# Kernel tuning notes

Hardware: AMD Instinct MI355X
Metric: run time of the kernel (lower is better)

## Reference

```python
import jax, jax.numpy as jnp
import numpy as np

DIM = 1024
HEADS = 16
DIM_HEAD = 64
INNER = HEADS * DIM_HEAD  # 1024
SCALE = DIM ** (-0.5)  # module scales by dim**-0.5 (not dim_head)


def setup_inputs() -> dict:
    key = jax.random.key(0)
    kx, kqkv, kwo, kbo = jax.random.split(key, 4)
    x = jax.random.normal(kx, (2, 2048, DIM), dtype=jnp.float32)
    W_qkv = jax.random.normal(kqkv, (DIM, 3 * INNER), dtype=jnp.float32) * (DIM ** -0.5)
    W_out = jax.random.normal(kwo, (INNER, DIM), dtype=jnp.float32) * (INNER ** -0.5)
    b_out = jax.random.normal(kbo, (DIM,), dtype=jnp.float32) * 0.01
    return {"x": x, "W_qkv": W_qkv, "W_out": W_out, "b_out": b_out}


def reference(x, W_qkv, W_out, b_out):
    b, n, _ = x.shape
    qkv = x @ W_qkv  # [b, n, 3*inner]
    q, k, v = jnp.split(qkv, 3, axis=-1)
    # [b, n, h*d] -> [b, h, n, d]
    reshape = lambda t: t.reshape(b, n, HEADS, DIM_HEAD).transpose(0, 2, 1, 3)
    q, k, v = reshape(q), reshape(k), reshape(v)
    dots = jnp.einsum('bhid,bhjd->bhij', q, k) * SCALE  # [b, h, n, n]
    attn = jax.nn.softmax(dots, axis=-1)
    out = jnp.einsum('bhij,bhjd->bhid', attn, v)  # [b, h, n, d]
    out = out.transpose(0, 2, 1, 3).reshape(b, n, INNER)
    return out @ W_out + b_out
```

## Files before the change

kernel.cpp:

```cpp
#include <hip/hip_runtime.h>

typedef __bf16 bf16x8 __attribute__((ext_vector_type(8)));
typedef __bf16 bf16x4 __attribute__((ext_vector_type(4)));
typedef float f32x4 __attribute__((ext_vector_type(4)));

__device__ __forceinline__ void async16(void* lds, const void* g) {
  __builtin_amdgcn_global_load_lds(
      (__attribute__((address_space(1))) unsigned int*)(g),
      (__attribute__((address_space(3))) unsigned int*)(lds), 16, 0, 0);
}

__device__ __forceinline__ int detect_block(const unsigned short* win, int* cnt_sh) {
  if (threadIdx.x == 0) *cnt_sh = 0;
  __syncthreads();
  int c = 0;
#pragma unroll
  for (int j = 0; j < 8; j++) {
    const unsigned short u = win[threadIdx.x * 8 + j];
    if (((u >> 7) & 0xFF) >= 0xC0) c++;
  }
  if (c) atomicAdd(cnt_sh, c);
  __syncthreads();
  return (*cnt_sh >= 64) ? 1 : 0;
}

__global__ void cvt_bf16(const void* __restrict__ src, __bf16* __restrict__ dst,
                         long n, int* __restrict__ flagp) {
  __shared__ int cnt;
  const long base = (long)blockIdx.x * 2048;
  const int f = detect_block((const unsigned short*)src + base, &cnt);
  if (blockIdx.x == 0 && threadIdx.x == 0) *flagp = f;
  const long i = base + threadIdx.x * 8;
  if (i >= n) return;
  if (f) {
    const float* s = (const float*)src;
#pragma unroll
    for (int j = 0; j < 8; j++) dst[i + j] = (__bf16)s[i + j];
  } else {
    *(bf16x8*)&dst[i] = *(const bf16x8*)((const __bf16*)src + i);
  }
}

__global__ __launch_bounds__(256) void transpose_both(
    const void* __restrict__ Wqkv, const void* __restrict__ Wout,
    __bf16* __restrict__ WqkvT, __bf16* __restrict__ WoutT)
{
  __shared__ __bf16 tile[64][65];
  __shared__ int cnt;
  const int bx = blockIdx.x;
  const void* in;  __bf16* out;  int R, C, tx;
  if (bx < 48) { in = Wqkv; out = WqkvT; R = 1024; C = 3072; tx = bx; }
  else         { in = Wout; out = WoutT; R = 1024; C = 1024; tx = bx - 48; }
  const int tc = tx * 64;
  const int tr = blockIdx.y * 64;
  const int f = detect_block((const unsigned short*)in + (long)(tr * C + tc), &cnt);
  const int t = threadIdx.x;
#pragma unroll
  for (int i = 0; i < 16; i++) {
    const int idx = t + 256 * i;
    const int r = idx >> 6, c = idx & 63;
    const long g = (long)(tr + r) * C + tc + c;
    tile[r][c] = f ? (__bf16)((const float*)in)[g] : ((const __bf16*)in)[g];
  }
  __syncthreads();
#pragma unroll
  for (int i = 0; i < 16; i++) {
    const int idx = t + 256 * i;
    const int r = idx >> 6, c = idx & 63;
    out[(long)(tc + r) * R + tr + c] = tile[c][r];
  }
}

__global__ __launch_bounds__(256, 2) void gemm_qkv(
    const __bf16* __restrict__ A, const __bf16* __restrict__ Bt,
    __bf16* __restrict__ Cqk, __bf16* __restrict__ Vt)
{
  __shared__ __bf16 As[128 * 32];
  __shared__ __bf16 Bs[128 * 32];
  const int t = threadIdx.x;
  const int l = t & 63;
  const int w = t >> 6;
  const int wr = w >> 1, wc = w & 1;
  const long m0 = (long)blockIdx.x * 128;
  const long n0 = (long)blockIdx.y * 128;
  const int K = 1024;

  const int srow = w * 16 + (l >> 2);
  const int skof = (l & 3) * 8;
  const __bf16* gA = A + (m0 + srow) * (long)K + skof;
  const __bf16* gB = Bt + (n0 + srow) * (long)K + skof;
  __bf16* lA = As + w * 512 + l * 8;
  __bf16* lB = Bs + w * 512 + l * 8;

  f32x4 acc[4][4] = {};

  for (int k0 = 0; k0 < K; k0 += 32) {
    __syncthreads();
    async16(lA,        gA);
    async16(lA + 2048, gA + 64 * (long)K);
    async16(lB,        gB);
    async16(lB + 2048, gB + 64 * (long)K);
    gA += 32; gB += 32;
    __syncthreads();

    bf16x8 af[4], bfr[4];
#pragma unroll
    for (int mi = 0; mi < 4; mi++)
      af[mi] = *(const bf16x8*)&As[(wr * 64 + mi * 16 + (l & 15)) * 32 + (l >> 4) * 8];
#pragma unroll
    for (int ni = 0; ni < 4; ni++)
      bfr[ni] = *(const bf16x8*)&Bs[(wc * 64 + ni * 16 + (l & 15)) * 32 + (l >> 4) * 8];
#pragma unroll
    for (int mi = 0; mi < 4; mi++)
#pragma unroll
      for (int ni = 0; ni < 4; ni++)
        acc[mi][ni] = __builtin_amdgcn_mfma_f32_16x16x32_bf16(af[mi], bfr[ni], acc[mi][ni], 0, 0, 0);
  }

  if (n0 < 2048) {
#pragma unroll
    for (int mi = 0; mi < 4; mi++)
#pragma unroll
      for (int ni = 0; ni < 4; ni++) {
        const long col = n0 + wc * 64 + ni * 16 + (l & 15);
#pragma unroll
        for (int r = 0; r < 4; r++) {
          const long row = m0 + wr * 64 + mi * 16 + (l >> 4) * 4 + r;
          Cqk[row * 2048 + col] = (__bf16)acc[mi][ni][r];
        }
      }
  } else {
    const int b = (int)(m0 >> 11);
    const int nb0 = (int)(m0 & 2047) + wr * 64 + (l >> 4) * 4;
#pragma unroll
    for (int mi = 0; mi < 4; mi++) {
      const int nb = nb0 + mi * 16;
#pragma unroll
      for (int ni = 0; ni < 4; ni++) {
        const int vcol = (int)(n0 - 2048) + wc * 64 + ni * 16 + (l & 15);
        const int bh = b * 16 + (vcol >> 6);
        const int d = vcol & 63;
        bf16x4 pk;
#pragma unroll
        for (int r = 0; r < 4; r++) pk[r] = (__bf16)acc[mi][ni][r];
        *(bf16x4*)&Vt[((long)bh * 64 + d) * 2048 + nb] = pk;
      }
    }
  }
}

__global__ __launch_bounds__(256, 4) void gemm_out(
    const __bf16* __restrict__ A, const __bf16* __restrict__ Bt,
    const void* __restrict__ bias_raw, void* __restrict__ C,
    const int* __restrict__ flagp)
{
  __shared__ __bf16 As[64 * 64];
  __shared__ __bf16 Bs[64 * 64];
  const int t = threadIdx.x;
  const int l = t & 63;
  const int w = t >> 6;
  const int wr = w >> 1, wc = w & 1;
  const long m0 = (long)blockIdx.x * 64;
  const long n0 = (long)blockIdx.y * 64;
  const int of = *flagp;
  const int K = 1024;

  const int srow = w * 8 + (l >> 3);
  const int sdof = ((l & 7) ^ (l >> 3)) * 8;
  const __bf16* gA = A + (m0 + srow) * (long)K + sdof;
  const __bf16* gB = Bt + (n0 + srow) * (long)K + sdof;
  __bf16* lA = As + w * 512 + l * 8;
  __bf16* lB = Bs + w * 512 + l * 8;

  f32x4 acc[2][2] = {};

  for (int k0 = 0; k0 < K; k0 += 64) {
    __syncthreads();
    async16(lA,        gA);
    async16(lA + 2048, gA + 32 * (long)K);
    async16(lB,        gB);
    async16(lB + 2048, gB + 32 * (long)K);
    gA += 64; gB += 64;
    __syncthreads();

#pragma unroll
    for (int kk = 0; kk < 2; kk++) {
      const int swz = ((kk * 4 + (l >> 4)) ^ (l & 7)) * 8;
      bf16x8 af[2], bfr[2];
#pragma unroll
      for (int mi = 0; mi < 2; mi++)
        af[mi] = *(const bf16x8*)&As[(wr * 32 + mi * 16 + (l & 15)) * 64 + swz];
#pragma unroll
      for (int ni = 0; ni < 2; ni++)
        bfr[ni] = *(const bf16x8*)&Bs[(wc * 32 + ni * 16 + (l & 15)) * 64 + swz];
#pragma unroll
      for (int mi = 0; mi < 2; mi++)
#pragma unroll
        for (int ni = 0; ni < 2; ni++)
          acc[mi][ni] = __builtin_amdgcn_mfma_f32_16x16x32_bf16(af[mi], bfr[ni], acc[mi][ni], 0, 0, 0);
    }
  }

#pragma unroll
  for (int mi = 0; mi < 2; mi++)
#pragma unroll
    for (int ni = 0; ni < 2; ni++) {
      const long col = n0 + wc * 32 + ni * 16 + (l & 15);
      const float bv = of ? ((const float*)bias_raw)[col]
                          : (float)((const __bf16*)bias_raw)[col];
#pragma unroll
      for (int r = 0; r < 4; r++) {
        const long row = m0 + wr * 32 + mi * 16 + (l >> 4) * 4 + r;
        const float val = acc[mi][ni][r] + bv;
        const long off = row * 1024 + col;
        if (of) ((float*)C)[off] = val;
        else    ((__bf16*)C)[off] = (__bf16)val;
      }
    }
}

#define EXP2_SCALE 0.045084439f

__global__ __launch_bounds__(256, 4) void attn_kernel(
    const __bf16* __restrict__ qk, const __bf16* __restrict__ Vt,
    __bf16* __restrict__ O)
{
  __shared__ __bf16 Qs[64 * 64];
  __shared__ __bf16 Ks[64 * 64];
  __shared__ __bf16 Vts[64 * 64];
  __shared__ __bf16 Ps[64 * 64];

  const int t = threadIdx.x;
  const int l = t & 63;
  const int w = t >> 6;
  const int qt = blockIdx.x;
  const int bh = blockIdx.y;
  const int b = bh >> 4, h = bh & 15;
  const long q_row0 = (long)b * 2048 + qt * 64;

  const int srow = w * 8 + (l >> 3);
  const int sdof = ((l & 7) ^ (l >> 3)) * 8;

  {
    const __bf16* g = qk + (q_row0 + srow) * 2048 + h * 64 + sdof;
    __bf16* lp = Qs + w * 512 + l * 8;
    async16(lp,        g);
    async16(lp + 2048, g + (long)32 * 2048);
  }

  const __bf16* gK = qk + ((long)b * 2048 + srow) * 2048 + 1024 + h * 64 + sdof;
  const __bf16* gV = Vt + ((long)bh * 64 + srow) * 2048 + sdof;
  __bf16* lK = Ks + w * 512 + l * 8;
  __bf16* lV = Vts + w * 512 + l * 8;

  __syncthreads();

  bf16x8 qf[2];
#pragma unroll
  for (int kk = 0; kk < 2; kk++)
    qf[kk] = *(const bf16x8*)&Qs[(w * 16 + (l & 15)) * 64 + (((kk * 4 + (l >> 4)) ^ (l & 7)) * 8)];

  f32x4 acc_o[4] = {};
  float l_i = 0.0f;

  for (int j0 = 0; j0 < 2048; j0 += 64) {
    __syncthreads();
    async16(lK,        gK);
    async16(lK + 2048, gK + 32 * 2048);
    async16(lV,        gV);
    async16(lV + 2048, gV + 32 * 2048);
    gK += (long)64 * 2048;
    gV += 64;
    __syncthreads();

    f32x4 s[4] = {};
#pragma unroll
    for (int kk = 0; kk < 2; kk++) {
      const int swz = ((kk * 4 + (l >> 4)) ^ (l & 7)) * 8;
#pragma unroll
      for (int ji = 0; ji < 4; ji++) {
        const bf16x8 ak = *(const bf16x8*)&Ks[(ji * 16 + (l & 15)) * 64 + swz];
        s[ji] = __builtin_amdgcn_mfma_f32_16x16x32_bf16(ak, qf[kk], s[ji], 0, 0, 0);
      }
    }

    float rs = 0.0f;
#pragma unroll
    for (int ji = 0; ji < 4; ji++)
#pragma unroll
      for (int r = 0; r < 4; r++) {
        const float p = exp2f(s[ji][r] * EXP2_SCALE);
        s[ji][r] = p;
        rs += p;
      }
    rs += __shfl_xor(rs, 16, 64);
    rs += __shfl_xor(rs, 32, 64);
    l_i += rs;

    {
      const int ibase = (w * 16 + (l & 15)) * 64;
      const int i7 = l & 7;
      const int sub = ((l >> 4) & 1) * 4;
      const int ghalf = l >> 5;
#pragma unroll
      for (int ji = 0; ji < 4; ji++) {
        bf16x4 pk;
#pragma unroll
        for (int r = 0; r < 4; r++) pk[r] = (__bf16)s[ji][r];
        const int g = ji * 2 + ghalf;
        *(bf16x4*)&Ps[ibase + ((g ^ i7) * 8) + sub] = pk;
      }
    }

#pragma unroll
    for (int kk = 0; kk < 2; kk++) {
      const int swz = ((kk * 4 + (l >> 4)) ^ (l & 7)) * 8;
      const bf16x8 ap = *(const bf16x8*)&Ps[(w * 16 + (l & 15)) * 64 + swz];
#pragma unroll
      for (int di = 0; di < 4; di++) {
        const bf16x8 bv = *(const bf16x8*)&Vts[(di * 16 + (l & 15)) * 64 + swz];
        acc_o[di] = __builtin_amdgcn_mfma_f32_16x16x32_bf16(ap, bv, acc_o[di], 0, 0, 0);
      }
    }
  }

#pragma unroll
  for (int rr = 0; rr < 4; rr++) {
    const float lsum = __shfl(l_i, ((l >> 4) << 2) + rr, 64);
    const float inv = 1.0f / lsum;
    const long row = q_row0 + w * 16 + (l >> 4) * 4 + rr;
#pragma unroll
    for (int di = 0; di < 4; di++) {
      const long col = (long)h * 64 + di * 16 + (l & 15);
      O[row * 1024 + col] = (__bf16)(acc_o[di][rr] * inv);
    }
  }
}

extern "C" void kernel_launch(void* const* d_in, const int* in_sizes, int n_in,
                              void* d_out, int out_size, void* d_ws, size_t ws_size,
                              hipStream_t stream) {
  const void* x    = d_in[0];
  const void* Wqkv = d_in[1];
  const void* Wout = d_in[2];
  const void* bout = d_in[3];

  char* ws = (char*)d_ws;
  int*    flagp = (int*)ws;
  __bf16* xb    = (__bf16*)(ws + 4096);
  __bf16* WqkvT = (__bf16*)(ws + 4096 +  8388608);
  __bf16* WoutT = (__bf16*)(ws + 4096 + 14680064);
  __bf16* qkbuf = (__bf16*)(ws + 4096 + 16777216);
  __bf16* VtBuf = (__bf16*)(ws + 4096 + 33554432);
  __bf16* Obuf  = (__bf16*)(ws + 4096 + 41943040);

  hipLaunchKernelGGL(cvt_bf16, dim3(2048), dim3(256), 0, stream,
                     x, xb, (long)4194304, flagp);
  hipLaunchKernelGGL(transpose_both, dim3(64, 16), dim3(256), 0, stream,
                     Wqkv, Wout, WqkvT, WoutT);
  hipLaunchKernelGGL(gemm_qkv, dim3(32, 24), dim3(256), 0, stream,
                     xb, WqkvT, qkbuf, VtBuf);
  hipLaunchKernelGGL(attn_kernel, dim3(32, 32), dim3(256), 0, stream,
                     qkbuf, VtBuf, Obuf);
  hipLaunchKernelGGL(gemm_out, dim3(64, 16), dim3(256), 0, stream,
                     Obuf, WoutT, bout, d_out, flagp);
}
```

Baseline: 206.8 us.

## Use 32x32 MFMA in attention, LDS-staged V transpose, larger gemm_out tiles

The attention kernel moves from 16x16x32 to 32x32x16 MFMA, with each wave computing a 32x32 quadrant of S and O. This adds a block barrier between writing P and reading it, and a cross-wave row-sum combine through LDS at the end. The V-transpose epilogue of gemm_qkv now stages the tile through padded shared memory so global writes are coalesced 16-byte stores. gemm_out switches to 128x64 tiles with a K step of 32 and a smaller grid, trading a different occupancy for more reuse per block.

```diff
diff --git a/kernel.cpp b/kernel.cpp
--- a/kernel.cpp
+++ b/kernel.cpp
@@ -3,6 +3,7 @@
 typedef __bf16 bf16x8 __attribute__((ext_vector_type(8)));
 typedef __bf16 bf16x4 __attribute__((ext_vector_type(4)));
 typedef float f32x4 __attribute__((ext_vector_type(4)));
+typedef float f32x16 __attribute__((ext_vector_type(16)));
 
 __device__ __forceinline__ void async16(void* lds, const void* g) {
   __builtin_amdgcn_global_load_lds(
@@ -75,8 +76,9 @@
     const __bf16* __restrict__ A, const __bf16* __restrict__ Bt,
     __bf16* __restrict__ Cqk, __bf16* __restrict__ Vt)
 {
-  __shared__ __bf16 As[128 * 32];
-  __shared__ __bf16 Bs[128 * 32];
+  __shared__ __bf16 smem[128 * 136];
+  __bf16* As = smem;
+  __bf16* Bs = smem + 4096;
   const int t = threadIdx.x;
   const int l = t & 63;
   const int w = t >> 6;
@@ -130,79 +132,81 @@
         }
       }
   } else {
+    __syncthreads();
+#pragma unroll
+    for (int mi = 0; mi < 4; mi++)
+#pragma unroll
+      for (int ni = 0; ni < 4; ni++) {
+        const int c = wc * 64 + ni * 16 + (l & 15);
+        const int r = wr * 64 + mi * 16 + (l >> 4) * 4;
+        bf16x4 pk;
+#pragma unroll
+        for (int k = 0; k < 4; k++) pk[k] = (__bf16)acc[mi][ni][k];
+        *(bf16x4*)&smem[c * 136 + r] = pk;
+      }
+    __syncthreads();
     const int b = (int)(m0 >> 11);
-    const int nb0 = (int)(m0 & 2047) + wr * 64 + (l >> 4) * 4;
-#pragma unroll
-    for (int mi = 0; mi < 4; mi++) {
-      const int nb = nb0 + mi * 16;
-#pragma unroll
-      for (int ni = 0; ni < 4; ni++) {
-        const int vcol = (int)(n0 - 2048) + wc * 64 + ni * 16 + (l & 15);
-        const int bh = b * 16 + (vcol >> 6);
-        const int d = vcol & 63;
-        bf16x4 pk;
-#pragma unroll
-        for (int r = 0; r < 4; r++) pk[r] = (__bf16)acc[mi][ni][r];
-        *(bf16x4*)&Vt[((long)bh * 64 + d) * 2048 + nb] = pk;
-      }
-    }
-  }
-}
-
-__global__ __launch_bounds__(256, 4) void gemm_out(
+    const int nbase = (int)(m0 & 2047);
+#pragma unroll
+    for (int i = 0; i < 8; i++) {
+      const int c = (t >> 4) + i * 16;
+      const int r8 = (t & 15) * 8;
+      const bf16x8 v = *(const bf16x8*)&smem[c * 136 + r8];
+      const int vcol = (int)(n0 - 2048) + c;
+      *(bf16x8*)&Vt[((long)(b * 16 + (vcol >> 6)) * 64 + (vcol & 63)) * 2048 + nbase + r8] = v;
+    }
+  }
+}
+
+__global__ __launch_bounds__(256, 2) void gemm_out(
     const __bf16* __restrict__ A, const __bf16* __restrict__ Bt,
     const void* __restrict__ bias_raw, void* __restrict__ C,
     const int* __restrict__ flagp)
 {
-  __shared__ __bf16 As[64 * 64];
-  __shared__ __bf16 Bs[64 * 64];
+  __shared__ __bf16 As[128 * 32];
+  __shared__ __bf16 Bs[64 * 32];
   const int t = threadIdx.x;
   const int l = t & 63;
   const int w = t >> 6;
   const int wr = w >> 1, wc = w & 1;
-  const long m0 = (long)blockIdx.x * 64;
+  const long m0 = (long)blockIdx.x * 128;
   const long n0 = (long)blockIdx.y * 64;
   const int of = *flagp;
   const int K = 1024;
 
-  const int srow = w * 8 + (l >> 3);
-  const int sdof = ((l & 7) ^ (l >> 3)) * 8;
-  const __bf16* gA = A + (m0 + srow) * (long)K + sdof;
-  const __bf16* gB = Bt + (n0 + srow) * (long)K + sdof;
+  const int srow = w * 16 + (l >> 2);
+  const int skof = (l & 3) * 8;
+  const __bf16* gA = A + (m0 + srow) * (long)K + skof;
+  const __bf16* gB = Bt + (n0 + srow) * (long)K + skof;
   __bf16* lA = As + w * 512 + l * 8;
   __bf16* lB = Bs + w * 512 + l * 8;
 
-  f32x4 acc[2][2] = {};
-
-  for (int k0 = 0; k0 < K; k0 += 64) {
+  f32x4 acc[4][2] = {};
+
+  for (int k0 = 0; k0 < K; k0 += 32) {
     __syncthreads();
     async16(lA,        gA);
-    async16(lA + 2048, gA + 32 * (long)K);
+    async16(lA + 2048, gA + 64 * (long)K);
     async16(lB,        gB);
-    async16(lB + 2048, gB + 32 * (long)K);
-    gA += 64; gB += 64;
-    __syncthreads();
-
-#pragma unroll
-    for (int kk = 0; kk < 2; kk++) {
-      const int swz = ((kk * 4 + (l >> 4)) ^ (l & 7)) * 8;
-      bf16x8 af[2], bfr[2];
-#pragma unroll
-      for (int mi = 0; mi < 2; mi++)
-        af[mi] = *(const bf16x8*)&As[(wr * 32 + mi * 16 + (l & 15)) * 64 + swz];
+    gA += 32; gB += 32;
+    __syncthreads();
+
+    bf16x8 af[4], bfr[2];
+#pragma unroll
+    for (int mi = 0; mi < 4; mi++)
+      af[mi] = *(const bf16x8*)&As[(wr * 64 + mi * 16 + (l & 15)) * 32 + (l >> 4) * 8];
+#pragma unroll
+    for (int ni = 0; ni < 2; ni++)
+      bfr[ni] = *(const bf16x8*)&Bs[(wc * 32 + ni * 16 + (l & 15)) * 32 + (l >> 4) * 8];
+#pragma unroll
+    for (int mi = 0; mi < 4; mi++)
 #pragma unroll
       for (int ni = 0; ni < 2; ni++)
-        bfr[ni] = *(const bf16x8*)&Bs[(wc * 32 + ni * 16 + (l & 15)) * 64 + swz];
-#pragma unroll
-      for (int mi = 0; mi < 2; mi++)
-#pragma unroll
-        for (int ni = 0; ni < 2; ni++)
-          acc[mi][ni] = __builtin_amdgcn_mfma_f32_16x16x32_bf16(af[mi], bfr[ni], acc[mi][ni], 0, 0, 0);
-    }
-  }
-
-#pragma unroll
-  for (int mi = 0; mi < 2; mi++)
+        acc[mi][ni] = __builtin_amdgcn_mfma_f32_16x16x32_bf16(af[mi], bfr[ni], acc[mi][ni], 0, 0, 0);
+  }
+
+#pragma unroll
+  for (int mi = 0; mi < 4; mi++)
 #pragma unroll
     for (int ni = 0; ni < 2; ni++) {
       const long col = n0 + wc * 32 + ni * 16 + (l & 15);
@@ -210,7 +214,7 @@
                           : (float)((const __bf16*)bias_raw)[col];
 #pragma unroll
       for (int r = 0; r < 4; r++) {
-        const long row = m0 + wr * 32 + mi * 16 + (l >> 4) * 4 + r;
+        const long row = m0 + wr * 64 + mi * 16 + (l >> 4) * 4 + r;
         const float val = acc[mi][ni][r] + bv;
         const long off = row * 1024 + col;
         if (of) ((float*)C)[off] = val;
@@ -233,6 +237,7 @@
   const int t = threadIdx.x;
   const int l = t & 63;
   const int w = t >> 6;
+  const int wi = w & 1, wj = w >> 1;
   const int qt = blockIdx.x;
   const int bh = blockIdx.y;
   const int b = bh >> 4, h = bh & 15;
@@ -255,12 +260,13 @@
 
   __syncthreads();
 
-  bf16x8 qf[2];
-#pragma unroll
-  for (int kk = 0; kk < 2; kk++)
-    qf[kk] = *(const bf16x8*)&Qs[(w * 16 + (l & 15)) * 64 + (((kk * 4 + (l >> 4)) ^ (l & 7)) * 8)];
-
-  f32x4 acc_o[4] = {};
+  const int i7 = l & 7;
+  bf16x8 qf[4];
+#pragma unroll
+  for (int kc = 0; kc < 4; kc++)
+    qf[kc] = *(const bf16x8*)&Qs[(wi * 32 + (l & 31)) * 64 + (((kc * 2 + (l >> 5)) ^ i7) * 8)];
+
+  f32x16 acc_o = {0,0,0,0,0,0,0,0,0,0,0,0,0,0,0,0};
   float l_i = 0.0f;
 
   for (int j0 = 0; j0 < 2048; j0 += 64) {
@@ -273,67 +279,58 @@
     gV += 64;
     __syncthreads();
 
-    f32x4 s[4] = {};
-#pragma unroll
-    for (int kk = 0; kk < 2; kk++) {
-      const int swz = ((kk * 4 + (l >> 4)) ^ (l & 7)) * 8;
-#pragma unroll
-      for (int ji = 0; ji < 4; ji++) {
-        const bf16x8 ak = *(const bf16x8*)&Ks[(ji * 16 + (l & 15)) * 64 + swz];
-        s[ji] = __builtin_amdgcn_mfma_f32_16x16x32_bf16(ak, qf[kk], s[ji], 0, 0, 0);
-      }
+    f32x16 st = {0,0,0,0,0,0,0,0,0,0,0,0,0,0,0,0};
+#pragma unroll
+    for (int kc = 0; kc < 4; kc++) {
+      const int swz = ((kc * 2 + (l >> 5)) ^ i7) * 8;
+      const bf16x8 ak = *(const bf16x8*)&Ks[(wj * 32 + (l & 31)) * 64 + swz];
+      st = __builtin_amdgcn_mfma_f32_32x32x16_bf16(ak, qf[kc], st, 0, 0, 0);
     }
 
     float rs = 0.0f;
 #pragma unroll
-    for (int ji = 0; ji < 4; ji++)
-#pragma unroll
-      for (int r = 0; r < 4; r++) {
-        const float p = exp2f(s[ji][r] * EXP2_SCALE);
-        s[ji][r] = p;
-        rs += p;
-      }
-    rs += __shfl_xor(rs, 16, 64);
+    for (int r = 0; r < 16; r++) {
+      const float p = exp2f(st[r] * EXP2_SCALE);
+      st[r] = p;
+      rs += p;
+    }
     rs += __shfl_xor(rs, 32, 64);
     l_i += rs;
 
     {
-      const int ibase = (w * 16 + (l & 15)) * 64;
-      const int i7 = l & 7;
-      const int sub = ((l >> 4) & 1) * 4;
-      const int ghalf = l >> 5;
-#pragma unroll
-      for (int ji = 0; ji < 4; ji++) {
+      const int ibase = (wi * 32 + (l & 31)) * 64;
+      const int sub = 4 * (l >> 5);
+#pragma unroll
+      for (int q = 0; q < 4; q++) {
         bf16x4 pk;
 #pragma unroll
-        for (int r = 0; r < 4; r++) pk[r] = (__bf16)s[ji][r];
-        const int g = ji * 2 + ghalf;
-        *(bf16x4*)&Ps[ibase + ((g ^ i7) * 8) + sub] = pk;
+        for (int r = 0; r < 4; r++) pk[r] = (__bf16)st[q * 4 + r];
+        const int gj = 4 * wj + q;
+        *(bf16x4*)&Ps[ibase + ((gj ^ i7) * 8) + sub] = pk;
       }
     }
-
-#pragma unroll
-    for (int kk = 0; kk < 2; kk++) {
-      const int swz = ((kk * 4 + (l >> 4)) ^ (l & 7)) * 8;
-      const bf16x8 ap = *(const bf16x8*)&Ps[(w * 16 + (l & 15)) * 64 + swz];
-#pragma unroll
-      for (int di = 0; di < 4; di++) {
-        const bf16x8 bv = *(const bf16x8*)&Vts[(di * 16 + (l & 15)) * 64 + swz];
-        acc_o[di] = __builtin_amdgcn_mfma_f32_16x16x32_bf16(ap, bv, acc_o[di], 0, 0, 0);
-      }
-    }
-  }
-
-#pragma unroll
-  for (int rr = 0; rr < 4; rr++) {
-    const float lsum = __shfl(l_i, ((l >> 4) << 2) + rr, 64);
-    const float inv = 1.0f / lsum;
-    const long row = q_row0 + w * 16 + (l >> 4) * 4 + rr;
-#pragma unroll
-    for (int di = 0; di < 4; di++) {
-      const long col = (long)h * 64 + di * 16 + (l & 15);
-      O[row * 1024 + col] = (__bf16)(acc_o[di][rr] * inv);
-    }
+    __syncthreads();
+
+#pragma unroll
+    for (int kc = 0; kc < 4; kc++) {
+      const int swz = ((kc * 2 + (l >> 5)) ^ i7) * 8;
+      const bf16x8 ap = *(const bf16x8*)&Ps[(wi * 32 + (l & 31)) * 64 + swz];
+      const bf16x8 bv = *(const bf16x8*)&Vts[(wj * 32 + (l & 31)) * 64 + swz];
+      acc_o = __builtin_amdgcn_mfma_f32_32x32x16_bf16(ap, bv, acc_o, 0, 0, 0);
+    }
+  }
+
+  __syncthreads();
+  float* lbuf = (float*)Ps;
+  if (l < 32) lbuf[w * 32 + l] = l_i;
+  __syncthreads();
+#pragma unroll
+  for (int r = 0; r < 16; r++) {
+    const int i_loc = (r & 3) + 8 * (r >> 2) + 4 * (l >> 5);
+    const float lsum = lbuf[wi * 32 + i_loc] + lbuf[(wi + 2) * 32 + i_loc];
+    const long row = q_row0 + wi * 32 + i_loc;
+    const long col = (long)h * 64 + wj * 32 + (l & 31);
+    O[row * 1024 + col] = (__bf16)(acc_o[r] / lsum);
   }
 }
 
@@ -362,6 +359,6 @@
                      xb, WqkvT, qkbuf, VtBuf);
   hipLaunchKernelGGL(attn_kernel, dim3(32, 32), dim3(256), 0, stream,
                      qkbuf, VtBuf, Obuf);
-  hipLaunchKernelGGL(gemm_out, dim3(64, 16), dim3(256), 0, stream,
+  hipLaunchKernelGGL(gemm_out, dim3(32, 16), dim3(256), 0, stream,
                      Obuf, WoutT, bout, d_out, flagp);
 }
```

Measured after the change: 207.2 us. About the same (+0.2%).
